# Optimization experiments

Measured on AMD Instinct MI355X. Metric: run time of the kernel, lower is better.

Reference implementation:

```python
import jax, jax.numpy as jnp
import numpy as np

EMBED = 1024

def setup_inputs() -> dict:
    key = jax.random.key(0)
    ks = jax.random.split(key, 7)
    s = 1.0 / np.sqrt(EMBED)  # ~ torch Linear default init scale
    x = jax.random.normal(ks[0], (4, 2048, EMBED), dtype=jnp.float32)
    Wq = jax.random.uniform(ks[1], (EMBED, EMBED), jnp.float32, -s, s)
    bq = jax.random.uniform(ks[2], (EMBED,), jnp.float32, -s, s)
    Wk = jax.random.uniform(ks[3], (EMBED, EMBED), jnp.float32, -s, s)
    bk = jax.random.uniform(ks[4], (EMBED,), jnp.float32, -s, s)
    Wv = jax.random.uniform(ks[5], (EMBED, EMBED), jnp.float32, -s, s)
    bv = jax.random.uniform(ks[6], (EMBED,), jnp.float32, -s, s)
    return {"x": x, "Wq": Wq, "bq": bq, "Wk": Wk, "bk": bk, "Wv": Wv, "bv": bv}

def reference(x, Wq, bq, Wk, bk, Wv, bv):
    # torch nn.Linear: y = x @ W.T + b
    q = jnp.einsum('bse,oe->bso', x, Wq) + bq
    k = jnp.einsum('bse,oe->bso', x, Wk) + bk
    v = jnp.einsum('bse,oe->bso', x, Wv) + bv
    scale = 1.0 / jnp.sqrt(jnp.float32(x.shape[-1]))
    scores = jnp.einsum('bqd,bkd->bqk', q, k) * scale  # [B,S,S]
    weights = jax.nn.softmax(scores, axis=-1)
    return jnp.einsum('bqk,bkd->bqd', weights, v)
```

## Files before the change

kernel.cpp:

```cpp
#include <hip/hip_runtime.h>
#include <stdint.h>

#define B_   4
#define S_   2048
#define E_   1024
#define MQKV (B_ * S_)
#define LDP  2112

typedef __bf16 bf16x8 __attribute__((ext_vector_type(8)));
typedef float f32x4 __attribute__((ext_vector_type(4)));
typedef unsigned short u16;
typedef unsigned int u32;

__device__ __forceinline__ u16 f2bf(float x) {
  union { float f; u32 u; } c; c.f = x;
  u32 r = (c.u + 0x7FFFu + ((c.u >> 16) & 1u)) >> 16;
  return (u16)r;
}

__global__ __launch_bounds__(256) void cvt_all(
    const float* __restrict__ x, const float* __restrict__ wq,
    const float* __restrict__ wk, const float* __restrict__ wv,
    u16* __restrict__ dst, float* __restrict__ Ls) {
  const int gid = blockIdx.x * 256 + threadIdx.x;
  if (gid < MQKV) Ls[gid] = 0.f;
  const int total = 2097152 + 786432;
  const int stride = gridDim.x * 256;
  for (int i = gid; i < total; i += stride) {
    float4 f;
    if (i < 2097152) {
      f = reinterpret_cast<const float4*>(x)[i];
    } else {
      const int j = i - 2097152;
      const int sel = j >> 18;
      const int r = j & 262143;
      const float* s = sel == 0 ? wq : (sel == 1 ? wk : wv);
      f = reinterpret_cast<const float4*>(s)[r];
    }
    ushort4 o;
    o.x = f2bf(f.x); o.y = f2bf(f.y); o.z = f2bf(f.z); o.w = f2bf(f.w);
    reinterpret_cast<ushort4*>(dst)[i] = o;
  }
}

#define GLOAD_LDS16(g, l)                                                      \
  __builtin_amdgcn_global_load_lds(                                            \
      (const __attribute__((address_space(1))) u32*)(g),                       \
      (__attribute__((address_space(3))) u32*)(l), 16, 0, 0)

template <int BN, int EPI>
__device__ __forceinline__ void gemm_body(
    const u16* __restrict__ A, const u16* __restrict__ Bt, void* __restrict__ Cv,
    const float* __restrict__ b0, const float* __restrict__ b1, float* __restrict__ Ls,
    int N, int K, float scale,
    long sA, long sB, long sC, long ldA, long ldB, long ldC, int gx, int gy) {
  constexpr int BM = 256;
  constexpr int NR = BN / 64;
  constexpr int L  = 2 + BN / 128;
  constexpr int BSLOT = BN * 32;

  __shared__ alignas(16) u16 lds[4 * BM * 32 + 4 * BSLOT];
  u16* lA = lds;
  u16* lB = lds + 4 * BM * 32;

  const int t = threadIdx.x;
  const int wv = t >> 6;
  const int ln = t & 63;
  const int wm = wv >> 2;
  const int wn = wv & 3;

  const int nwg = gridDim.x;
  int id = blockIdx.x;
  id = (id & 7) * (nwg >> 3) + (id >> 3);
  const int pz = gx * gy;
  const int z = id / pz;
  const int r2 = id - z * pz;
  const int by = r2 / gx;
  const int bx = r2 - by * gx;
  const int bm = by * BM;
  const int bn = bx * BN;

  A += (size_t)z * sA;
  Bt += (size_t)z * sB;

  const int srow = t >> 2;
  const int g0 = (t & 3) ^ ((srow >> 1) & 3);
  const u16* gA0 = A + (size_t)(bm + srow) * ldA + g0 * 8;
  const u16* gA1 = gA0 + (size_t)128 * ldA;
  const u16* gB0 = Bt + (size_t)(bn + srow) * ldB + g0 * 8;
  const u16* gB1 = gB0 + (size_t)128 * ldB;

  auto STAGE = [&](int u) {
    const int s = u & 3;
    const int ko = u * 32;
    GLOAD_LDS16(gA0 + ko, lA + s * 8192 + wv * 512);
    GLOAD_LDS16(gA1 + ko, lA + s * 8192 + 4096 + wv * 512);
    GLOAD_LDS16(gB0 + ko, lB + s * BSLOT + wv * 512);
    if constexpr (BN == 256) GLOAD_LDS16(gB1 + ko, lB + s * BSLOT + 4096 + wv * 512);
  };

  const int lrow = ln & 15;
  const int g = ln >> 4;
  const int aR = wm * 128 + lrow;
  const int aOff = aR * 32 + (g ^ ((aR >> 1) & 3)) * 8;
  const int bR = wn * (BN / 4) + lrow;
  const int bOff = bR * 32 + (g ^ ((bR >> 1) & 3)) * 8;

  f32x4 acc[8][NR] = {};
  const int T = K >> 5;

  bf16x8 afA[8], afB[8], bgA[NR], bgB[NR];

#define RD_A(DST, TILE) do { const u16* _p = lA + ((TILE) & 3) * 8192 + aOff;  \
  _Pragma("unroll") for (int _i = 0; _i < 8; ++_i)                             \
    DST[_i] = *reinterpret_cast<const bf16x8*>(_p + _i * 512); } while (0)
#define RD_B(DST, TILE) do { const u16* _p = lB + ((TILE) & 3) * BSLOT + bOff; \
  _Pragma("unroll") for (int _j = 0; _j < NR; ++_j)                            \
    DST[_j] = *reinterpret_cast<const bf16x8*>(_p + _j * 512); } while (0)
#define DO_MFMA(AF, BG) do { __builtin_amdgcn_s_setprio(1);                    \
  _Pragma("unroll") for (int _i = 0; _i < 8; ++_i)                             \
  _Pragma("unroll") for (int _j = 0; _j < NR; ++_j)                            \
    acc[_i][_j] = __builtin_amdgcn_mfma_f32_16x16x32_bf16(AF[_i], BG[_j],      \
                                                          acc[_i][_j], 0, 0, 0);\
  __builtin_amdgcn_s_setprio(0); } while (0)
#define VM_GATE(COND) do {                                                     \
  if (COND) { asm volatile("s_waitcnt vmcnt(%0)" :: "n"(L) : "memory"); }      \
  else { asm volatile("s_waitcnt vmcnt(0)" ::: "memory"); }                    \
  __builtin_amdgcn_s_barrier(); asm volatile("" ::: "memory"); } while (0)

  STAGE(0); STAGE(1); STAGE(2);
  asm volatile("s_waitcnt vmcnt(%0)" :: "n"(L) : "memory");
  __builtin_amdgcn_s_barrier();
  asm volatile("" ::: "memory");

  if constexpr (NR == 2) { RD_A(afA, 0); RD_B(bgA, 0); }
  else                   { RD_B(bgA, 0); }

  for (int tt = 0; tt < T; tt += 2) {
    if (tt + 3 < T) STAGE(tt + 3);
    if constexpr (NR == 2) { RD_A(afB, tt + 1); RD_B(bgB, tt + 1); DO_MFMA(afA, bgA); }
    else                   { RD_A(afA, tt); RD_B(bgB, tt + 1);     DO_MFMA(afA, bgA); }
    VM_GATE(tt + 3 < T);

    if (tt + 4 < T) STAGE(tt + 4);
    if constexpr (NR == 2) {
      if (tt + 2 < T) { RD_A(afA, tt + 2); RD_B(bgA, tt + 2); }
      DO_MFMA(afB, bgB);
    } else {
      RD_A(afA, tt + 1);
      if (tt + 2 < T) RD_B(bgA, tt + 2);
      DO_MFMA(afA, bgB);
    }
    VM_GATE(tt + 4 < T);
  }
#undef RD_A
#undef RD_B
#undef DO_MFMA
#undef VM_GATE

  const int r0 = (ln >> 4) * 4;
  const int c0 = ln & 15;
  if constexpr (EPI == 2) {
#pragma unroll
    for (int i = 0; i < 8; ++i) {
#pragma unroll
      for (int ii = 0; ii < 4; ++ii) {
        const int row = bm + wm * 128 + i * 16 + r0 + ii;
        float s = 0.f;
#pragma unroll
        for (int j = 0; j < NR; ++j) {
          const int col = bn + wn * (BN / 4) + j * 16 + c0;
          const float vex = __expf(acc[i][j][ii] * scale);
          ((u16*)Cv)[(size_t)z * sC + (size_t)row * ldC + col] = f2bf(vex);
          s += vex;
        }
        s += __shfl_xor(s, 1); s += __shfl_xor(s, 2);
        s += __shfl_xor(s, 4); s += __shfl_xor(s, 8);
        if ((ln & 15) == 0) unsafeAtomicAdd(&Ls[z * 2048 + row], s);
      }
    }
  } else {
#pragma unroll
    for (int i = 0; i < 8; ++i) {
#pragma unroll
      for (int j = 0; j < NR; ++j) {
        const int col = bn + wn * (BN / 4) + j * 16 + c0;
#pragma unroll
        for (int ii = 0; ii < 4; ++ii) {
          const int row = bm + wm * 128 + i * 16 + r0 + ii;
          float v = acc[i][j][ii];
          if constexpr (EPI == 0) {
            const int sel = col >> 10;
            const int cc = col & 1023;
            const float bb = sel == 0 ? b0[cc] : b1[cc];
            ((u16*)Cv)[(size_t)sel * 8388608 + (size_t)row * 1024 + cc] = f2bf(v + bb);
          } else {
            ((u16*)Cv)[(size_t)z * sC + (size_t)row * ldC + col] = f2bf(v + b0[row]);
          }
        }
      }
    }
  }
}

__global__ __launch_bounds__(512, 2) void qkproj_k(
    const u16* __restrict__ A, const u16* __restrict__ Bt, void* __restrict__ Cv,
    const float* __restrict__ b0, const float* __restrict__ b1,
    int N, int K, float scale, long sA, long sB, long sC,
    long ldA, long ldB, long ldC, int gx, int gy) {
  gemm_body<256, 0>(A, Bt, Cv, b0, b1, nullptr, N, K, scale, sA, sB, sC, ldA, ldB, ldC, gx, gy);
}
__global__ __launch_bounds__(512, 2) void vproj_k(
    const u16* __restrict__ A, const u16* __restrict__ Bt, void* __restrict__ Cv,
    const float* __restrict__ b0, const float* __restrict__ b1,
    int N, int K, float scale, long sA, long sB, long sC,
    long ldA, long ldB, long ldC, int gx, int gy) {
  gemm_body<128, 1>(A, Bt, Cv, b0, b1, nullptr, N, K, scale, sA, sB, sC, ldA, ldB, ldC, gx, gy);
}
__global__ __launch_bounds__(512, 2) void qkt_k(
    const u16* __restrict__ A, const u16* __restrict__ Bt, void* __restrict__ Cv,
    float* __restrict__ Ls,
    int N, int K, float scale, long sA, long sB, long sC,
    long ldA, long ldB, long ldC, int gx, int gy) {
  gemm_body<256, 2>(A, Bt, Cv, nullptr, nullptr, Ls, N, K, scale, sA, sB, sC, ldA, ldB, ldC, gx, gy);
}

__global__ __launch_bounds__(512, 2) void pv_k(
    const u16* __restrict__ Pm, const u16* __restrict__ vt,
    float* __restrict__ out, const float* __restrict__ Ls) {
  __shared__ alignas(16) u16 lA[3 * 16384];
  __shared__ alignas(16) u16 lB[3 * 8192];
  const int t = threadIdx.x;
  const int wv = t >> 6, ln = t & 63;
  const int wm = wv >> 2, wn = wv & 3;

  int id = blockIdx.x;
  id = (id & 7) * 32 + (id >> 3);
  const int z = id >> 6;
  const int r2 = id & 63;
  const int by = r2 >> 3, bx = r2 & 7;
  const int bm = by * 256, bn = bx * 128;

  const u16* A = Pm + (size_t)z * 2048 * LDP;
  const u16* Bt = vt + (size_t)z * 1024 * LDP;

  const int sr = t >> 3;
  const int scw = ((t & 7) ^ (sr & 7)) * 8;
  const u16* Ab = A + (size_t)(bm + sr) * LDP + scw;
  const u16* Bb = Bt + (size_t)(bn + sr) * LDP + scw;

#define PSTG(u) do { const int _s = (u) % 3; const long _ko = (long)(u) * 64;  \
  _Pragma("unroll") for (int _q = 0; _q < 4; ++_q)                             \
    GLOAD_LDS16(Ab + (size_t)_q * 64 * LDP + _ko, lA + _s * 16384 + _q * 4096 + t * 8); \
  _Pragma("unroll") for (int _q = 0; _q < 2; ++_q)                             \
    GLOAD_LDS16(Bb + (size_t)_q * 64 * LDP + _ko, lB + _s * 8192 + _q * 4096 + t * 8);  \
} while (0)

  const int lrow = ln & 15, g = ln >> 4;
  const int ch0 = (g ^ (lrow & 7)) * 8;
  const int ch1 = ((4 | g) ^ (lrow & 7)) * 8;

  f32x4 acc[8][2] = {};

  PSTG(0); PSTG(1);
  asm volatile("s_waitcnt vmcnt(6)" ::: "memory");
  __builtin_amdgcn_s_barrier();
  asm volatile("" ::: "memory");

  for (int u = 0; u < 32; ++u) {
    if (u + 2 < 32) PSTG(u + 2);
    const int s = u % 3;
    const u16* pA = lA + s * 16384 + lrow * 64;
    const u16* pB = lB + s * 8192 + lrow * 64;
    bf16x8 a[8][2], b[2][2];
#pragma unroll
    for (int mf = 0; mf < 8; ++mf) {
      const int ro = (wm * 128 + mf * 16) * 64;
      a[mf][0] = *reinterpret_cast<const bf16x8*>(pA + ro + ch0);
      a[mf][1] = *reinterpret_cast<const bf16x8*>(pA + ro + ch1);
    }
#pragma unroll
    for (int nf = 0; nf < 2; ++nf) {
      const int ro = (wn * 32 + nf * 16) * 64;
      b[nf][0] = *reinterpret_cast<const bf16x8*>(pB + ro + ch0);
      b[nf][1] = *reinterpret_cast<const bf16x8*>(pB + ro + ch1);
    }
    __builtin_amdgcn_s_setprio(1);
#pragma unroll
    for (int ks = 0; ks < 2; ++ks)
#pragma unroll
      for (int mf = 0; mf < 8; ++mf)
#pragma unroll
        for (int nf = 0; nf < 2; ++nf)
          acc[mf][nf] = __builtin_amdgcn_mfma_f32_16x16x32_bf16(
              a[mf][ks], b[nf][ks], acc[mf][nf], 0, 0, 0);
    __builtin_amdgcn_s_setprio(0);
    if (u < 31) {
      if (u + 2 < 32) { asm volatile("s_waitcnt vmcnt(6)" ::: "memory"); }
      else            { asm volatile("s_waitcnt vmcnt(0)" ::: "memory"); }
      __builtin_amdgcn_s_barrier();
      asm volatile("" ::: "memory");
    }
  }
#undef PSTG

  const int r0 = g * 4, c0 = lrow;
#pragma unroll
  for (int mf = 0; mf < 8; ++mf) {
#pragma unroll
    for (int ii = 0; ii < 4; ++ii) {
      const int row = bm + wm * 128 + mf * 16 + r0 + ii;
      const float inv = 1.0f / Ls[z * 2048 + row];
#pragma unroll
      for (int nf = 0; nf < 2; ++nf) {
        const int col = bn + wn * 32 + nf * 16 + c0;
        out[((size_t)z * 2048 + row) * 1024 + col] = acc[mf][nf][ii] * inv;
      }
    }
  }
}

extern "C" void kernel_launch(void* const* d_in, const int* in_sizes, int n_in,
                              void* d_out, int out_size, void* d_ws, size_t ws_size,
                              hipStream_t stream) {
  const float* x = (const float*)d_in[0];
  const float* Wq = (const float*)d_in[1];
  const float* bq = (const float*)d_in[2];
  const float* Wk = (const float*)d_in[3];
  const float* bk = (const float*)d_in[4];
  const float* Wv = (const float*)d_in[5];
  const float* bv = (const float*)d_in[6];
  float* out = (float*)d_out;

  const size_t xE = 8388608, wE = 3145728, qE = 8388608;
  const size_t vtE = (size_t)4 * 1024 * LDP;
  const size_t PmE = (size_t)4 * 2048 * LDP;
  const size_t need = (xE + wE + 2 * qE + vtE + PmE) * 2 + (size_t)MQKV * 4;
  if (ws_size < need) {
    hipMemsetAsync(d_out, 0, (size_t)out_size * sizeof(float), stream);
    return;
  }
  u16* xb = (u16*)d_ws;
  u16* wqkv = xb + xE;
  u16* qb = wqkv + wE;
  u16* vt = qb + 2 * qE;
  u16* Pm = vt + vtE;
  float* Ls = (float*)(Pm + PmE);

  cvt_all<<<2048, 256, 0, stream>>>(x, Wq, Wk, Wv, xb, Ls);

  qkproj_k<<<256, 512, 0, stream>>>(
      xb, wqkv, qb, bq, bk, 2048, E_, 1.f,
      0, 0, 0, E_, E_, 1024, 8, 32);

  vproj_k<<<256, 512, 0, stream>>>(
      wqkv + 2 * (size_t)E_ * E_, xb, vt, bv, nullptr, 2048, E_, 1.f,
      0, (long)S_ * E_, (long)1024 * LDP, E_, E_, LDP, 16, 4);

  qkt_k<<<256, 512, 0, stream>>>(
      qb, qb + 8388608, Pm, Ls, 2048, E_, 0.03125f,
      (long)S_ * 1024, (long)S_ * 1024, (long)2048 * LDP, 1024, 1024, LDP, 8, 8);

  pv_k<<<256, 512, 0, stream>>>(Pm, vt, out, Ls);
}
```

Measured before the change: 160.3 us.

## Unify all GEMMs on 256x128 K64 tile body and compute softmax sums separately

Measured after the change: 194.1 us. 1.21x slower.

```diff
diff --git a/kernel.cpp b/kernel.cpp
--- a/kernel.cpp
+++ b/kernel.cpp
@@ -17,13 +17,16 @@
   u32 r = (c.u + 0x7FFFu + ((c.u >> 16) & 1u)) >> 16;
   return (u16)r;
 }
+__device__ __forceinline__ float bf2f(u16 h) {
+  union { u32 u; float f; } c; c.u = ((u32)h) << 16;
+  return c.f;
+}
 
 __global__ __launch_bounds__(256) void cvt_all(
     const float* __restrict__ x, const float* __restrict__ wq,
     const float* __restrict__ wk, const float* __restrict__ wv,
-    u16* __restrict__ dst, float* __restrict__ Ls) {
+    u16* __restrict__ dst) {
   const int gid = blockIdx.x * 256 + threadIdx.x;
-  if (gid < MQKV) Ls[gid] = 0.f;
   const int total = 2097152 + 786432;
   const int stride = gridDim.x * 256;
   for (int i = gid; i < total; i += stride) {
@@ -48,26 +51,17 @@
       (const __attribute__((address_space(1))) u32*)(g),                       \
       (__attribute__((address_space(3))) u32*)(l), 16, 0, 0)
 
-template <int BN, int EPI>
-__device__ __forceinline__ void gemm_body(
-    const u16* __restrict__ A, const u16* __restrict__ Bt, void* __restrict__ Cv,
-    const float* __restrict__ b0, const float* __restrict__ b1, float* __restrict__ Ls,
-    int N, int K, float scale,
-    long sA, long sB, long sC, long ldA, long ldB, long ldC, int gx, int gy) {
-  constexpr int BM = 256;
-  constexpr int NR = BN / 64;
-  constexpr int L  = 2 + BN / 128;
-  constexpr int BSLOT = BN * 32;
-
-  __shared__ alignas(16) u16 lds[4 * BM * 32 + 4 * BSLOT];
-  u16* lA = lds;
-  u16* lB = lds + 4 * BM * 32;
-
+template <int EPI>
+__device__ __forceinline__ void g64_body(
+    const u16* __restrict__ A, const u16* __restrict__ Bt, void* __restrict__ Cv,
+    const float* __restrict__ b0, const float* __restrict__ b1,
+    int K, float scale, long sA, long sB, long sC,
+    long ldA, long ldB, long ldC, int gx, int gy) {
+  __shared__ alignas(16) u16 lA[3 * 16384];
+  __shared__ alignas(16) u16 lB[3 * 8192];
   const int t = threadIdx.x;
-  const int wv = t >> 6;
-  const int ln = t & 63;
-  const int wm = wv >> 2;
-  const int wn = wv & 3;
+  const int wv = t >> 6, ln = t & 63;
+  const int wm = wv >> 2, wn = wv & 3;
 
   const int nwg = gridDim.x;
   int id = blockIdx.x;
@@ -77,183 +71,21 @@
   const int r2 = id - z * pz;
   const int by = r2 / gx;
   const int bx = r2 - by * gx;
-  const int bm = by * BM;
-  const int bn = bx * BN;
+  const int bm = by * 256, bn = bx * 128;
 
   A += (size_t)z * sA;
   Bt += (size_t)z * sB;
 
-  const int srow = t >> 2;
-  const int g0 = (t & 3) ^ ((srow >> 1) & 3);
-  const u16* gA0 = A + (size_t)(bm + srow) * ldA + g0 * 8;
-  const u16* gA1 = gA0 + (size_t)128 * ldA;
-  const u16* gB0 = Bt + (size_t)(bn + srow) * ldB + g0 * 8;
-  const u16* gB1 = gB0 + (size_t)128 * ldB;
-
-  auto STAGE = [&](int u) {
-    const int s = u & 3;
-    const int ko = u * 32;
-    GLOAD_LDS16(gA0 + ko, lA + s * 8192 + wv * 512);
-    GLOAD_LDS16(gA1 + ko, lA + s * 8192 + 4096 + wv * 512);
-    GLOAD_LDS16(gB0 + ko, lB + s * BSLOT + wv * 512);
-    if constexpr (BN == 256) GLOAD_LDS16(gB1 + ko, lB + s * BSLOT + 4096 + wv * 512);
-  };
-
-  const int lrow = ln & 15;
-  const int g = ln >> 4;
-  const int aR = wm * 128 + lrow;
-  const int aOff = aR * 32 + (g ^ ((aR >> 1) & 3)) * 8;
-  const int bR = wn * (BN / 4) + lrow;
-  const int bOff = bR * 32 + (g ^ ((bR >> 1) & 3)) * 8;
-
-  f32x4 acc[8][NR] = {};
-  const int T = K >> 5;
-
-  bf16x8 afA[8], afB[8], bgA[NR], bgB[NR];
-
-#define RD_A(DST, TILE) do { const u16* _p = lA + ((TILE) & 3) * 8192 + aOff;  \
-  _Pragma("unroll") for (int _i = 0; _i < 8; ++_i)                             \
-    DST[_i] = *reinterpret_cast<const bf16x8*>(_p + _i * 512); } while (0)
-#define RD_B(DST, TILE) do { const u16* _p = lB + ((TILE) & 3) * BSLOT + bOff; \
-  _Pragma("unroll") for (int _j = 0; _j < NR; ++_j)                            \
-    DST[_j] = *reinterpret_cast<const bf16x8*>(_p + _j * 512); } while (0)
-#define DO_MFMA(AF, BG) do { __builtin_amdgcn_s_setprio(1);                    \
-  _Pragma("unroll") for (int _i = 0; _i < 8; ++_i)                             \
-  _Pragma("unroll") for (int _j = 0; _j < NR; ++_j)                            \
-    acc[_i][_j] = __builtin_amdgcn_mfma_f32_16x16x32_bf16(AF[_i], BG[_j],      \
-                                                          acc[_i][_j], 0, 0, 0);\
-  __builtin_amdgcn_s_setprio(0); } while (0)
-#define VM_GATE(COND) do {                                                     \
-  if (COND) { asm volatile("s_waitcnt vmcnt(%0)" :: "n"(L) : "memory"); }      \
-  else { asm volatile("s_waitcnt vmcnt(0)" ::: "memory"); }                    \
-  __builtin_amdgcn_s_barrier(); asm volatile("" ::: "memory"); } while (0)
-
-  STAGE(0); STAGE(1); STAGE(2);
-  asm volatile("s_waitcnt vmcnt(%0)" :: "n"(L) : "memory");
-  __builtin_amdgcn_s_barrier();
-  asm volatile("" ::: "memory");
-
-  if constexpr (NR == 2) { RD_A(afA, 0); RD_B(bgA, 0); }
-  else                   { RD_B(bgA, 0); }
-
-  for (int tt = 0; tt < T; tt += 2) {
-    if (tt + 3 < T) STAGE(tt + 3);
-    if constexpr (NR == 2) { RD_A(afB, tt + 1); RD_B(bgB, tt + 1); DO_MFMA(afA, bgA); }
-    else                   { RD_A(afA, tt); RD_B(bgB, tt + 1);     DO_MFMA(afA, bgA); }
-    VM_GATE(tt + 3 < T);
-
-    if (tt + 4 < T) STAGE(tt + 4);
-    if constexpr (NR == 2) {
-      if (tt + 2 < T) { RD_A(afA, tt + 2); RD_B(bgA, tt + 2); }
-      DO_MFMA(afB, bgB);
-    } else {
-      RD_A(afA, tt + 1);
-      if (tt + 2 < T) RD_B(bgA, tt + 2);
-      DO_MFMA(afA, bgB);
-    }
-    VM_GATE(tt + 4 < T);
-  }
-#undef RD_A
-#undef RD_B
-#undef DO_MFMA
-#undef VM_GATE
-
-  const int r0 = (ln >> 4) * 4;
-  const int c0 = ln & 15;
-  if constexpr (EPI == 2) {
-#pragma unroll
-    for (int i = 0; i < 8; ++i) {
-#pragma unroll
-      for (int ii = 0; ii < 4; ++ii) {
-        const int row = bm + wm * 128 + i * 16 + r0 + ii;
-        float s = 0.f;
-#pragma unroll
-        for (int j = 0; j < NR; ++j) {
-          const int col = bn + wn * (BN / 4) + j * 16 + c0;
-          const float vex = __expf(acc[i][j][ii] * scale);
-          ((u16*)Cv)[(size_t)z * sC + (size_t)row * ldC + col] = f2bf(vex);
-          s += vex;
-        }
-        s += __shfl_xor(s, 1); s += __shfl_xor(s, 2);
-        s += __shfl_xor(s, 4); s += __shfl_xor(s, 8);
-        if ((ln & 15) == 0) unsafeAtomicAdd(&Ls[z * 2048 + row], s);
-      }
-    }
-  } else {
-#pragma unroll
-    for (int i = 0; i < 8; ++i) {
-#pragma unroll
-      for (int j = 0; j < NR; ++j) {
-        const int col = bn + wn * (BN / 4) + j * 16 + c0;
-#pragma unroll
-        for (int ii = 0; ii < 4; ++ii) {
-          const int row = bm + wm * 128 + i * 16 + r0 + ii;
-          float v = acc[i][j][ii];
-          if constexpr (EPI == 0) {
-            const int sel = col >> 10;
-            const int cc = col & 1023;
-            const float bb = sel == 0 ? b0[cc] : b1[cc];
-            ((u16*)Cv)[(size_t)sel * 8388608 + (size_t)row * 1024 + cc] = f2bf(v + bb);
-          } else {
-            ((u16*)Cv)[(size_t)z * sC + (size_t)row * ldC + col] = f2bf(v + b0[row]);
-          }
-        }
-      }
-    }
-  }
-}
-
-__global__ __launch_bounds__(512, 2) void qkproj_k(
-    const u16* __restrict__ A, const u16* __restrict__ Bt, void* __restrict__ Cv,
-    const float* __restrict__ b0, const float* __restrict__ b1,
-    int N, int K, float scale, long sA, long sB, long sC,
-    long ldA, long ldB, long ldC, int gx, int gy) {
-  gemm_body<256, 0>(A, Bt, Cv, b0, b1, nullptr, N, K, scale, sA, sB, sC, ldA, ldB, ldC, gx, gy);
-}
-__global__ __launch_bounds__(512, 2) void vproj_k(
-    const u16* __restrict__ A, const u16* __restrict__ Bt, void* __restrict__ Cv,
-    const float* __restrict__ b0, const float* __restrict__ b1,
-    int N, int K, float scale, long sA, long sB, long sC,
-    long ldA, long ldB, long ldC, int gx, int gy) {
-  gemm_body<128, 1>(A, Bt, Cv, b0, b1, nullptr, N, K, scale, sA, sB, sC, ldA, ldB, ldC, gx, gy);
-}
-__global__ __launch_bounds__(512, 2) void qkt_k(
-    const u16* __restrict__ A, const u16* __restrict__ Bt, void* __restrict__ Cv,
-    float* __restrict__ Ls,
-    int N, int K, float scale, long sA, long sB, long sC,
-    long ldA, long ldB, long ldC, int gx, int gy) {
-  gemm_body<256, 2>(A, Bt, Cv, nullptr, nullptr, Ls, N, K, scale, sA, sB, sC, ldA, ldB, ldC, gx, gy);
-}
-
-__global__ __launch_bounds__(512, 2) void pv_k(
-    const u16* __restrict__ Pm, const u16* __restrict__ vt,
-    float* __restrict__ out, const float* __restrict__ Ls) {
-  __shared__ alignas(16) u16 lA[3 * 16384];
-  __shared__ alignas(16) u16 lB[3 * 8192];
-  const int t = threadIdx.x;
-  const int wv = t >> 6, ln = t & 63;
-  const int wm = wv >> 2, wn = wv & 3;
-
-  int id = blockIdx.x;
-  id = (id & 7) * 32 + (id >> 3);
-  const int z = id >> 6;
-  const int r2 = id & 63;
-  const int by = r2 >> 3, bx = r2 & 7;
-  const int bm = by * 256, bn = bx * 128;
-
-  const u16* A = Pm + (size_t)z * 2048 * LDP;
-  const u16* Bt = vt + (size_t)z * 1024 * LDP;
-
   const int sr = t >> 3;
   const int scw = ((t & 7) ^ (sr & 7)) * 8;
-  const u16* Ab = A + (size_t)(bm + sr) * LDP + scw;
-  const u16* Bb = Bt + (size_t)(bn + sr) * LDP + scw;
+  const u16* Ab = A + (size_t)(bm + sr) * ldA + scw;
+  const u16* Bb = Bt + (size_t)(bn + sr) * ldB + scw;
 
 #define PSTG(u) do { const int _s = (u) % 3; const long _ko = (long)(u) * 64;  \
   _Pragma("unroll") for (int _q = 0; _q < 4; ++_q)                             \
-    GLOAD_LDS16(Ab + (size_t)_q * 64 * LDP + _ko, lA + _s * 16384 + _q * 4096 + t * 8); \
+    GLOAD_LDS16(Ab + (size_t)_q * 64 * ldA + _ko, lA + _s * 16384 + _q * 4096 + t * 8); \
   _Pragma("unroll") for (int _q = 0; _q < 2; ++_q)                             \
-    GLOAD_LDS16(Bb + (size_t)_q * 64 * LDP + _ko, lB + _s * 8192 + _q * 4096 + t * 8);  \
+    GLOAD_LDS16(Bb + (size_t)_q * 64 * ldB + _ko, lB + _s * 8192 + _q * 4096 + t * 8);  \
 } while (0)
 
   const int lrow = ln & 15, g = ln >> 4;
@@ -261,14 +93,15 @@
   const int ch1 = ((4 | g) ^ (lrow & 7)) * 8;
 
   f32x4 acc[8][2] = {};
+  const int T = K >> 6;
 
   PSTG(0); PSTG(1);
   asm volatile("s_waitcnt vmcnt(6)" ::: "memory");
   __builtin_amdgcn_s_barrier();
   asm volatile("" ::: "memory");
 
-  for (int u = 0; u < 32; ++u) {
-    if (u + 2 < 32) PSTG(u + 2);
+  for (int u = 0; u < T; ++u) {
+    if (u + 2 < T) PSTG(u + 2);
     const int s = u % 3;
     const u16* pA = lA + s * 16384 + lrow * 64;
     const u16* pB = lB + s * 8192 + lrow * 64;
@@ -295,9 +128,9 @@
           acc[mf][nf] = __builtin_amdgcn_mfma_f32_16x16x32_bf16(
               a[mf][ks], b[nf][ks], acc[mf][nf], 0, 0, 0);
     __builtin_amdgcn_s_setprio(0);
-    if (u < 31) {
-      if (u + 2 < 32) { asm volatile("s_waitcnt vmcnt(6)" ::: "memory"); }
-      else            { asm volatile("s_waitcnt vmcnt(0)" ::: "memory"); }
+    if (u < T - 1) {
+      if (u + 2 < T) { asm volatile("s_waitcnt vmcnt(6)" ::: "memory"); }
+      else           { asm volatile("s_waitcnt vmcnt(0)" ::: "memory"); }
       __builtin_amdgcn_s_barrier();
       asm volatile("" ::: "memory");
     }
@@ -310,14 +143,74 @@
 #pragma unroll
     for (int ii = 0; ii < 4; ++ii) {
       const int row = bm + wm * 128 + mf * 16 + r0 + ii;
-      const float inv = 1.0f / Ls[z * 2048 + row];
 #pragma unroll
       for (int nf = 0; nf < 2; ++nf) {
         const int col = bn + wn * 32 + nf * 16 + c0;
-        out[((size_t)z * 2048 + row) * 1024 + col] = acc[mf][nf][ii] * inv;
+        float v = acc[mf][nf][ii];
+        if constexpr (EPI == 0) {
+          const int sel = col >> 10;
+          const int cc = col & 1023;
+          const float bb = sel == 0 ? b0[cc] : b1[cc];
+          ((u16*)Cv)[(size_t)sel * 8388608 + (size_t)row * 1024 + cc] = f2bf(v + bb);
+        } else if constexpr (EPI == 1) {
+          ((u16*)Cv)[(size_t)z * sC + (size_t)row * ldC + col] = f2bf(v + b0[row]);
+        } else if constexpr (EPI == 2) {
+          ((u16*)Cv)[(size_t)z * sC + (size_t)row * ldC + col] = f2bf(__expf(v * scale));
+        } else {
+          ((float*)Cv)[(size_t)z * sC + (size_t)row * ldC + col] = v * b0[z * 2048 + row];
+        }
       }
     }
   }
+}
+
+__global__ __launch_bounds__(512, 2) void qkproj_k(
+    const u16* __restrict__ A, const u16* __restrict__ Bt, void* __restrict__ Cv,
+    const float* __restrict__ b0, const float* __restrict__ b1,
+    int K, float scale, long sA, long sB, long sC,
+    long ldA, long ldB, long ldC, int gx, int gy) {
+  g64_body<0>(A, Bt, Cv, b0, b1, K, scale, sA, sB, sC, ldA, ldB, ldC, gx, gy);
+}
+__global__ __launch_bounds__(512, 2) void vproj_k(
+    const u16* __restrict__ A, const u16* __restrict__ Bt, void* __restrict__ Cv,
+    const float* __restrict__ b0, const float* __restrict__ b1,
+    int K, float scale, long sA, long sB, long sC,
+    long ldA, long ldB, long ldC, int gx, int gy) {
+  g64_body<1>(A, Bt, Cv, b0, b1, K, scale, sA, sB, sC, ldA, ldB, ldC, gx, gy);
+}
+__global__ __launch_bounds__(512, 2) void qkt_k(
+    const u16* __restrict__ A, const u16* __restrict__ Bt, void* __restrict__ Cv,
+    const float* __restrict__ b0, const float* __restrict__ b1,
+    int K, float scale, long sA, long sB, long sC,
+    long ldA, long ldB, long ldC, int gx, int gy) {
+  g64_body<2>(A, Bt, Cv, b0, b1, K, scale, sA, sB, sC, ldA, ldB, ldC, gx, gy);
+}
+__global__ __launch_bounds__(512, 2) void pv_k(
+    const u16* __restrict__ A, const u16* __restrict__ Bt, void* __restrict__ Cv,
+    const float* __restrict__ b0, const float* __restrict__ b1,
+    int K, float scale, long sA, long sB, long sC,
+    long ldA, long ldB, long ldC, int gx, int gy) {
+  g64_body<3>(A, Bt, Cv, b0, b1, K, scale, sA, sB, sC, ldA, ldB, ldC, gx, gy);
+}
+
+__global__ __launch_bounds__(256) void row_invsum(const u16* __restrict__ P,
+                                                  float* __restrict__ invL) {
+  const int row = blockIdx.x * 4 + (threadIdx.x >> 6);
+  const int ln = threadIdx.x & 63;
+  const u16* p = P + (size_t)row * LDP + ln * 32;
+  float s = 0.f;
+#pragma unroll
+  for (int q = 0; q < 4; ++q) {
+    uint4 r = reinterpret_cast<const uint4*>(p)[q];
+    u32 w[4] = {r.x, r.y, r.z, r.w};
+#pragma unroll
+    for (int k = 0; k < 4; ++k) {
+      s += bf2f((u16)(w[k] & 0xffffu));
+      s += bf2f((u16)(w[k] >> 16));
+    }
+  }
+  for (int o = 1; o < 64; o <<= 1) s += __shfl_xor(s, o);
+  if (ln == 0) invL[row] = 1.0f / s;
 }
 
 extern "C" void kernel_launch(void* const* d_in, const int* in_sizes, int n_in,
@@ -345,21 +238,25 @@
   u16* qb = wqkv + wE;
   u16* vt = qb + 2 * qE;
   u16* Pm = vt + vtE;
-  float* Ls = (float*)(Pm + PmE);
-
-  cvt_all<<<2048, 256, 0, stream>>>(x, Wq, Wk, Wv, xb, Ls);
-
-  qkproj_k<<<256, 512, 0, stream>>>(
-      xb, wqkv, qb, bq, bk, 2048, E_, 1.f,
-      0, 0, 0, E_, E_, 1024, 8, 32);
+  float* invL = (float*)(Pm + PmE);
+
+  cvt_all<<<2048, 256, 0, stream>>>(x, Wq, Wk, Wv, xb);
+
+  qkproj_k<<<512, 512, 0, stream>>>(
+      xb, wqkv, qb, bq, bk, E_, 1.f,
+      0, 0, 0, E_, E_, 1024, 16, 32);
 
   vproj_k<<<256, 512, 0, stream>>>(
-      wqkv + 2 * (size_t)E_ * E_, xb, vt, bv, nullptr, 2048, E_, 1.f,
+      wqkv + 2 * (size_t)E_ * E_, xb, vt, bv, nullptr, E_, 1.f,
       0, (long)S_ * E_, (long)1024 * LDP, E_, E_, LDP, 16, 4);
 
-  qkt_k<<<256, 512, 0, stream>>>(
-      qb, qb + 8388608, Pm, Ls, 2048, E_, 0.03125f,
-      (long)S_ * 1024, (long)S_ * 1024, (long)2048 * LDP, 1024, 1024, LDP, 8, 8);
-
-  pv_k<<<256, 512, 0, stream>>>(Pm, vt, out, Ls);
-}
+  qkt_k<<<512, 512, 0, stream>>>(
+      qb, qb + 8388608, Pm, nullptr, nullptr, E_, 0.03125f,
+      (long)S_ * 1024, (long)S_ * 1024, (long)2048 * LDP, 1024, 1024, LDP, 16, 8);
+
+  row_invsum<<<B_ * S_ / 4, 256, 0, stream>>>(Pm, invL);
+
+  pv_k<<<256, 512, 0, stream>>>(
+      Pm, vt, out, invL, nullptr, S_, 1.f,
+      (long)2048 * LDP, (long)1024 * LDP, (long)S_ * E_, LDP, LDP, 1024, 8, 8);
+}
```

## Replace atomic row-sum softmax with separate row-sum kernel and pad Q/K rows

Applied to the files above, without the earlier changes.

Result: no change. 160.5 us (+0.1%).

```diff
diff --git a/kernel.cpp b/kernel.cpp
--- a/kernel.cpp
+++ b/kernel.cpp
@@ -5,6 +5,7 @@
 #define S_   2048
 #define E_   1024
 #define MQKV (B_ * S_)
+#define LDQ  1056
 #define LDP  2112
 
 typedef __bf16 bf16x8 __attribute__((ext_vector_type(8)));
@@ -17,13 +18,16 @@
   u32 r = (c.u + 0x7FFFu + ((c.u >> 16) & 1u)) >> 16;
   return (u16)r;
 }
+__device__ __forceinline__ float bf2f(u16 h) {
+  union { u32 u; float f; } c; c.u = ((u32)h) << 16;
+  return c.f;
+}
 
 __global__ __launch_bounds__(256) void cvt_all(
     const float* __restrict__ x, const float* __restrict__ wq,
     const float* __restrict__ wk, const float* __restrict__ wv,
-    u16* __restrict__ dst, float* __restrict__ Ls) {
+    u16* __restrict__ dst) {
   const int gid = blockIdx.x * 256 + threadIdx.x;
-  if (gid < MQKV) Ls[gid] = 0.f;
   const int total = 2097152 + 786432;
   const int stride = gridDim.x * 256;
   for (int i = gid; i < total; i += stride) {
@@ -51,7 +55,7 @@
 template <int BN, int EPI>
 __device__ __forceinline__ void gemm_body(
     const u16* __restrict__ A, const u16* __restrict__ Bt, void* __restrict__ Cv,
-    const float* __restrict__ b0, const float* __restrict__ b1, float* __restrict__ Ls,
+    const float* __restrict__ b0, const float* __restrict__ b1,
     int N, int K, float scale,
     long sA, long sB, long sC, long ldA, long ldB, long ldC, int gx, int gy) {
   constexpr int BM = 256;
@@ -160,43 +164,24 @@
 
   const int r0 = (ln >> 4) * 4;
   const int c0 = ln & 15;
-  if constexpr (EPI == 2) {
-#pragma unroll
-    for (int i = 0; i < 8; ++i) {
+#pragma unroll
+  for (int i = 0; i < 8; ++i) {
+#pragma unroll
+    for (int j = 0; j < NR; ++j) {
+      const int col = bn + wn * (BN / 4) + j * 16 + c0;
 #pragma unroll
       for (int ii = 0; ii < 4; ++ii) {
         const int row = bm + wm * 128 + i * 16 + r0 + ii;
-        float s = 0.f;
-#pragma unroll
-        for (int j = 0; j < NR; ++j) {
-          const int col = bn + wn * (BN / 4) + j * 16 + c0;
-          const float vex = __expf(acc[i][j][ii] * scale);
-          ((u16*)Cv)[(size_t)z * sC + (size_t)row * ldC + col] = f2bf(vex);
-          s += vex;
-        }
-        s += __shfl_xor(s, 1); s += __shfl_xor(s, 2);
-        s += __shfl_xor(s, 4); s += __shfl_xor(s, 8);
-        if ((ln & 15) == 0) unsafeAtomicAdd(&Ls[z * 2048 + row], s);
-      }
-    }
-  } else {
-#pragma unroll
-    for (int i = 0; i < 8; ++i) {
-#pragma unroll
-      for (int j = 0; j < NR; ++j) {
-        const int col = bn + wn * (BN / 4) + j * 16 + c0;
-#pragma unroll
-        for (int ii = 0; ii < 4; ++ii) {
-          const int row = bm + wm * 128 + i * 16 + r0 + ii;
-          float v = acc[i][j][ii];
-          if constexpr (EPI == 0) {
-            const int sel = col >> 10;
-            const int cc = col & 1023;
-            const float bb = sel == 0 ? b0[cc] : b1[cc];
-            ((u16*)Cv)[(size_t)sel * 8388608 + (size_t)row * 1024 + cc] = f2bf(v + bb);
-          } else {
-            ((u16*)Cv)[(size_t)z * sC + (size_t)row * ldC + col] = f2bf(v + b0[row]);
-          }
+        float v = acc[i][j][ii];
+        if constexpr (EPI == 0) {
+          const int sel = col >> 10;
+          const int cc = col & 1023;
+          const float bb = sel == 0 ? b0[cc] : b1[cc];
+          ((u16*)Cv)[(size_t)sel * 8650752 + (size_t)row * LDQ + cc] = f2bf(v + bb);
+        } else if constexpr (EPI == 1) {
+          ((u16*)Cv)[(size_t)z * sC + (size_t)row * ldC + col] = f2bf(v + b0[row]);
+        } else {
+          ((u16*)Cv)[(size_t)z * sC + (size_t)row * ldC + col] = f2bf(__expf(v * scale));
         }
       }
     }
@@ -208,26 +193,46 @@
     const float* __restrict__ b0, const float* __restrict__ b1,
     int N, int K, float scale, long sA, long sB, long sC,
     long ldA, long ldB, long ldC, int gx, int gy) {
-  gemm_body<256, 0>(A, Bt, Cv, b0, b1, nullptr, N, K, scale, sA, sB, sC, ldA, ldB, ldC, gx, gy);
+  gemm_body<256, 0>(A, Bt, Cv, b0, b1, N, K, scale, sA, sB, sC, ldA, ldB, ldC, gx, gy);
 }
 __global__ __launch_bounds__(512, 2) void vproj_k(
     const u16* __restrict__ A, const u16* __restrict__ Bt, void* __restrict__ Cv,
     const float* __restrict__ b0, const float* __restrict__ b1,
     int N, int K, float scale, long sA, long sB, long sC,
     long ldA, long ldB, long ldC, int gx, int gy) {
-  gemm_body<128, 1>(A, Bt, Cv, b0, b1, nullptr, N, K, scale, sA, sB, sC, ldA, ldB, ldC, gx, gy);
+  gemm_body<128, 1>(A, Bt, Cv, b0, b1, N, K, scale, sA, sB, sC, ldA, ldB, ldC, gx, gy);
 }
 __global__ __launch_bounds__(512, 2) void qkt_k(
     const u16* __restrict__ A, const u16* __restrict__ Bt, void* __restrict__ Cv,
-    float* __restrict__ Ls,
+    const float* __restrict__ b0, const float* __restrict__ b1,
     int N, int K, float scale, long sA, long sB, long sC,
     long ldA, long ldB, long ldC, int gx, int gy) {
-  gemm_body<256, 2>(A, Bt, Cv, nullptr, nullptr, Ls, N, K, scale, sA, sB, sC, ldA, ldB, ldC, gx, gy);
+  gemm_body<256, 2>(A, Bt, Cv, b0, b1, N, K, scale, sA, sB, sC, ldA, ldB, ldC, gx, gy);
+}
+
+__global__ __launch_bounds__(256) void row_invsum(const u16* __restrict__ P,
+                                                  float* __restrict__ invL) {
+  const int row = blockIdx.x * 4 + (threadIdx.x >> 6);
+  const int ln = threadIdx.x & 63;
+  const u16* p = P + (size_t)row * LDP + ln * 32;
+  float s = 0.f;
+#pragma unroll
+  for (int q = 0; q < 4; ++q) {
+    uint4 r = reinterpret_cast<const uint4*>(p)[q];
+    u32 w[4] = {r.x, r.y, r.z, r.w};
+#pragma unroll
+    for (int k = 0; k < 4; ++k) {
+      s += bf2f((u16)(w[k] & 0xffffu));
+      s += bf2f((u16)(w[k] >> 16));
+    }
+  }
+  for (int o = 1; o < 64; o <<= 1) s += __shfl_xor(s, o);
+  if (ln == 0) invL[row] = 1.0f / s;
 }
 
 __global__ __launch_bounds__(512, 2) void pv_k(
     const u16* __restrict__ Pm, const u16* __restrict__ vt,
-    float* __restrict__ out, const float* __restrict__ Ls) {
+    float* __restrict__ out, const float* __restrict__ invL) {
   __shared__ alignas(16) u16 lA[3 * 16384];
   __shared__ alignas(16) u16 lB[3 * 8192];
   const int t = threadIdx.x;
@@ -310,7 +315,7 @@
 #pragma unroll
     for (int ii = 0; ii < 4; ++ii) {
       const int row = bm + wm * 128 + mf * 16 + r0 + ii;
-      const float inv = 1.0f / Ls[z * 2048 + row];
+      const float inv = invL[z * 2048 + row];
 #pragma unroll
       for (int nf = 0; nf < 2; ++nf) {
         const int col = bn + wn * 32 + nf * 16 + c0;
@@ -332,7 +337,8 @@
   const float* bv = (const float*)d_in[6];
   float* out = (float*)d_out;
 
-  const size_t xE = 8388608, wE = 3145728, qE = 8388608;
+  const size_t xE = 8388608, wE = 3145728;
+  const size_t qE = (size_t)8192 * LDQ;
   const size_t vtE = (size_t)4 * 1024 * LDP;
   const size_t PmE = (size_t)4 * 2048 * LDP;
   const size_t need = (xE + wE + 2 * qE + vtE + PmE) * 2 + (size_t)MQKV * 4;
@@ -345,21 +351,23 @@
   u16* qb = wqkv + wE;
   u16* vt = qb + 2 * qE;
   u16* Pm = vt + vtE;
-  float* Ls = (float*)(Pm + PmE);
-
-  cvt_all<<<2048, 256, 0, stream>>>(x, Wq, Wk, Wv, xb, Ls);
+  float* invL = (float*)(Pm + PmE);
+
+  cvt_all<<<2048, 256, 0, stream>>>(x, Wq, Wk, Wv, xb);
 
   qkproj_k<<<256, 512, 0, stream>>>(
       xb, wqkv, qb, bq, bk, 2048, E_, 1.f,
-      0, 0, 0, E_, E_, 1024, 8, 32);
+      0, 0, 0, E_, E_, LDQ, 8, 32);
 
   vproj_k<<<256, 512, 0, stream>>>(
       wqkv + 2 * (size_t)E_ * E_, xb, vt, bv, nullptr, 2048, E_, 1.f,
       0, (long)S_ * E_, (long)1024 * LDP, E_, E_, LDP, 16, 4);
 
   qkt_k<<<256, 512, 0, stream>>>(
-      qb, qb + 8388608, Pm, Ls, 2048, E_, 0.03125f,
-      (long)S_ * 1024, (long)S_ * 1024, (long)2048 * LDP, 1024, 1024, LDP, 8, 8);
-
-  pv_k<<<256, 512, 0, stream>>>(Pm, vt, out, Ls);
-}
+      qb, qb + qE, Pm, nullptr, nullptr, 2048, E_, 0.03125f,
+      (long)S_ * LDQ, (long)S_ * LDQ, (long)2048 * LDP, LDQ, LDQ, LDP, 8, 8);
+
+  row_invsum<<<B_ * S_ / 4, 256, 0, stream>>>(Pm, invL);
+
+  pv_k<<<256, 512, 0, stream>>>(Pm, vt, out, invL);
+}
```
